# Optimization experiments

Hardware: AMD Instinct MI355X
Metric: run time of the kernel (lower is better)

## Reference

```python
import jax, jax.numpy as jnp
import numpy as np

P_CLAMP = 10.0      # opt.p
OUTPUT_SCALE = 0.1  # opt.output_scale
S_LR = 0.1          # s_lr passed to step()
R_DIM, C_DIM, HID, NLAYERS = 8192, 2048, 20, 2


def _lstm_one_step(x, h0, c0, layers):
    # x: (B, 1) single-time-step input; h0, c0: (NLAYERS, B, HID)
    # torch gate order: i, f, g, o
    inp = x
    for l, (Wih, Whh, bih, bhh) in enumerate(layers):
        gates = inp @ Wih.T + bih + h0[l] @ Whh.T + bhh  # (B, 4H)
        i, f, g, o = jnp.split(gates, 4, axis=-1)
        c = jax.nn.sigmoid(f) * c0[l] + jax.nn.sigmoid(i) * jnp.tanh(g)
        inp = jax.nn.sigmoid(o) * jnp.tanh(c)
    return inp  # last-layer hidden state (B, HID)


def _orth_proj(M, G):
    # tangent projection on the Stiefel manifold
    A = M.T @ G                      # (c, c)
    A_sym = 0.5 * (A + A.T)
    return G - M @ A_sym


def _retraction(M, P):
    Q, R = jnp.linalg.qr(M + P)      # reduced QR, M+P is (r, c), r >= c
    sign = jnp.sign(jnp.sign(jnp.diagonal(R)) + 0.5)  # maps 0 -> +1
    return Q * sign[None, :]


def _log_sign_diag(gram_diag):
    # diagonal of LogAndSign_Preprocess_Gradient: clamp(log|x|/p, -1, 1)
    return jnp.clip(jnp.log(jnp.abs(gram_diag)) / P_CLAMP, -1.0, 1.0)[:, None]


def reference(s, s_grad, L_h0, L_c0, R_h0, R_c0, L_before, R_before,
              W_ih0, W_hh0, b_ih0, b_hh0, W_ih1, W_hh1, b_ih1, b_hh1,
              L_W, L_b, R_W, R_b):
    s0 = s.shape[0]
    M = s.reshape(s0, -1).T                   # (r, c)
    M_grad = s_grad.reshape(s0, -1).T * S_LR  # (r, c)
    r, c = M.shape
    G = _orth_proj(M, M_grad)
    # only the diagonals of GG^T/c and G^TG/r are ever used by the preprocess
    ggt_diag = jnp.sum(G * G, axis=1) / c     # (r,)
    gtg_diag = jnp.sum(G * G, axis=0) / r     # (c,)
    layers = [(W_ih0, W_hh0, b_ih0, b_hh0), (W_ih1, W_hh1, b_ih1, b_hh1)]
    hl = _lstm_one_step(_log_sign_diag(ggt_diag), L_h0, L_c0, layers)  # (r, H)
    hr = _lstm_one_step(_log_sign_diag(gtg_diag), R_h0, R_c0, layers)  # (c, H)
    l_ = (hl @ L_W.T + L_b).squeeze(-1) * OUTPUT_SCALE
    l_ = l_ - l_.mean() + 1.0
    r_ = (hr @ R_W.T + R_b).squeeze(-1) * OUTPUT_SCALE
    r_ = r_ - r_.mean() + 1.0
    Lv = jnp.maximum(l_, L_before)            # diag matrices stored as vectors
    Rv = jnp.maximum(r_, R_before)
    P = Lv[:, None] * G * Rv[None, :]         # L @ G @ R with diagonal L, R
    P = _orth_proj(M, P)
    new_s = _retraction(M, -P).T.reshape(s.shape)
    return new_s


def setup_inputs() -> dict:
    key = jax.random.key(0)
    ks = jax.random.split(key, 16)
    H4 = 4 * HID
    return {
        "s": jax.random.normal(ks[0], (C_DIM, R_DIM), jnp.float32) * 0.02,
        "s_grad": jax.random.normal(ks[1], (C_DIM, R_DIM), jnp.float32) * 0.02,
        "L_h0": jax.random.normal(ks[2], (NLAYERS, R_DIM, HID), jnp.float32) * 0.1,
        "L_c0": jax.random.normal(ks[3], (NLAYERS, R_DIM, HID), jnp.float32) * 0.1,
        "R_h0": jax.random.normal(ks[4], (NLAYERS, C_DIM, HID), jnp.float32) * 0.1,
        "R_c0": jax.random.normal(ks[5], (NLAYERS, C_DIM, HID), jnp.float32) * 0.1,
        "L_before": jnp.ones((R_DIM,), jnp.float32),
        "R_before": jnp.ones((C_DIM,), jnp.float32),
        "W_ih0": jax.random.normal(ks[6], (H4, 1), jnp.float32) * 0.2,
        "W_hh0": jax.random.normal(ks[7], (H4, HID), jnp.float32) * 0.2,
        "b_ih0": jax.random.normal(ks[8], (H4,), jnp.float32) * 0.1,
        "b_hh0": jax.random.normal(ks[9], (H4,), jnp.float32) * 0.1,
        "W_ih1": jax.random.normal(ks[10], (H4, HID), jnp.float32) * 0.2,
        "W_hh1": jax.random.normal(ks[11], (H4, HID), jnp.float32) * 0.2,
        "b_ih1": jax.random.normal(ks[12], (H4,), jnp.float32) * 0.1,
        "b_hh1": jax.random.normal(ks[13], (H4,), jnp.float32) * 0.1,
        "L_W": jax.random.normal(ks[14], (1, HID), jnp.float32) * 0.2,
        "L_b": jnp.zeros((1,), jnp.float32),
        "R_W": jax.random.normal(ks[15], (1, HID), jnp.float32) * 0.2,
        "R_b": jnp.zeros((1,), jnp.float32),
    }
```

## Files before the change

### kernel.cpp

```cpp
#include <hip/hip_runtime.h>
#include <math.h>

#define RD 8192
#define CD 2048

typedef _Float16 f16x8 __attribute__((ext_vector_type(8)));
typedef _Float16 f16x4 __attribute__((ext_vector_type(4)));
typedef float    f32x4 __attribute__((ext_vector_type(4)));

#define GLOBAL_AS __attribute__((address_space(1)))
#define LDS_AS    __attribute__((address_space(3)))

__global__ __launch_bounds__(512, 2) void gemm_nt_f16(
    const _Float16* __restrict__ A, const _Float16* __restrict__ B,
    float* __restrict__ Cp, _Float16* __restrict__ Of16,
    const float* __restrict__ Dg, const _Float16* __restrict__ Eg,
    int M, int N, int K, int ksplit, float beta, float gamma, float sgn)
{
  __shared__ __align__(1024) _Float16 As[2][256 * 32];
  __shared__ __align__(1024) _Float16 Bs[2][256 * 32];
  const int tid = threadIdx.x;
  const int wave = tid >> 6, lane = tid & 63;
  const int wy = wave >> 2, wx = wave & 3;
  const int bi = blockIdx.y * 256, bj = blockIdx.x * 256;
  const int kchunk = K / ksplit;
  const long k0 = (long)blockIdx.z * kchunk;

  f32x4 acc[8][4];
#pragma unroll
  for (int i = 0; i < 8; ++i)
#pragma unroll
    for (int j = 0; j < 4; ++j) acc[i][j] = (f32x4){0.f, 0.f, 0.f, 0.f};

  const int srow = wave * 16 + (lane >> 2);
  const int skof = (lane & 3) * 8;
  const _Float16* aA = A + (long)(bi + srow) * K + k0 + skof;
  const _Float16* aB = B + (long)(bj + srow) * K + k0 + skof;
  const int ldso = wave * 16 * 32;

#define STAGE(buf, kt)                                                         \
  {                                                                            \
    _Float16* lA = &As[buf][ldso];                                             \
    _Float16* lB = &Bs[buf][ldso];                                             \
    _Pragma("unroll")                                                          \
    for (int q = 0; q < 2; ++q) {                                              \
      __builtin_amdgcn_global_load_lds(                                        \
          (const GLOBAL_AS unsigned int*)(aA + (long)q * 128 * K + (kt)),      \
          (LDS_AS unsigned int*)(lA + q * 128 * 32), 16, 0, 0);                \
      __builtin_amdgcn_global_load_lds(                                        \
          (const GLOBAL_AS unsigned int*)(aB + (long)q * 128 * K + (kt)),      \
          (LDS_AS unsigned int*)(lB + q * 128 * 32), 16, 0, 0);                \
    }                                                                          \
  }

  const int fr = lane & 15;
  const int fk = (lane >> 4) * 8;

  STAGE(0, 0);
  __syncthreads();
  int cur = 0;
  for (int kt = 0; kt < kchunk; kt += 32) {
    if (kt + 32 < kchunk) STAGE(cur ^ 1, kt + 32);

    f16x8 af[8], bf[4];
#pragma unroll
    for (int t = 0; t < 8; ++t)
      af[t] = *(const f16x8*)(&As[cur][(wy * 128 + t * 16 + fr) * 32 + fk]);
#pragma unroll
    for (int t = 0; t < 4; ++t)
      bf[t] = *(const f16x8*)(&Bs[cur][(wx * 64 + t * 16 + fr) * 32 + fk]);
#pragma unroll
    for (int mt = 0; mt < 8; ++mt)
#pragma unroll
      for (int nt = 0; nt < 4; ++nt)
        acc[mt][nt] = __builtin_amdgcn_mfma_f32_16x16x32_f16(af[mt], bf[nt], acc[mt][nt], 0, 0, 0);

    __syncthreads();
    cur ^= 1;
  }
#undef STAGE

  const int quad = lane >> 4, fc = lane & 15;
  if (Cp) {
#pragma unroll
    for (int mt = 0; mt < 8; ++mt)
#pragma unroll
      for (int nt = 0; nt < 4; ++nt) {
        const int col = bj + wx * 64 + nt * 16 + fc;
#pragma unroll
        for (int reg = 0; reg < 4; ++reg) {
          const int row = bi + wy * 128 + mt * 16 + quad * 4 + reg;
          atomicAdd(&Cp[(long)row * N + col], acc[mt][nt][reg]);
        }
      }
  } else {
#pragma unroll
    for (int mt = 0; mt < 8; ++mt)
#pragma unroll
      for (int nt = 0; nt < 4; ++nt) {
        const int col = bj + wx * 64 + nt * 16 + fc;
#pragma unroll
        for (int reg = 0; reg < 4; ++reg) {
          const int row = bi + wy * 128 + mt * 16 + quad * 4 + reg;
          const long off = (long)row * N + col;
          float v = sgn * acc[mt][nt][reg];
          if (Dg) v += beta * Dg[off];
          if (Eg) v += gamma * (float)Eg[off];
          Of16[off] = (_Float16)v;
        }
      }
  }
}

__global__ __launch_bounds__(256) void sym_combine(
    const float* __restrict__ Cp, float* __restrict__ out, int n, int nsplit, float scale)
{
  __shared__ float Ts[64][68];
  const int tid = threadIdx.x;
  const int tx = tid & 15, ty = tid >> 4;
  const int bi = blockIdx.y * 64, bj = blockIdx.x * 64;
  float acc[4][4];
#pragma unroll
  for (int i = 0; i < 4; ++i)
#pragma unroll
    for (int j = 0; j < 4; ++j) acc[i][j] = 0.f;

  for (int s = 0; s < nsplit; ++s) {
    const float* C = Cp + (long)s * n * n;
#pragma unroll
    for (int i = 0; i < 4; ++i) {
      float4 v = *(const float4*)(C + (long)(bi + ty * 4 + i) * n + bj + tx * 4);
      acc[i][0] += v.x; acc[i][1] += v.y; acc[i][2] += v.z; acc[i][3] += v.w;
    }
    __syncthreads();
#pragma unroll
    for (int i = 0; i < 4; ++i) {
      float4 w = *(const float4*)(C + (long)(bj + ty * 4 + i) * n + bi + tx * 4);
      *(float4*)&Ts[ty * 4 + i][tx * 4] = w;
    }
    __syncthreads();
#pragma unroll
    for (int i = 0; i < 4; ++i)
#pragma unroll
      for (int j = 0; j < 4; ++j) acc[i][j] += Ts[tx * 4 + j][ty * 4 + i];
  }
#pragma unroll
  for (int i = 0; i < 4; ++i) {
    float4 v; v.x = scale * acc[i][0]; v.y = scale * acc[i][1]; v.z = scale * acc[i][2]; v.w = scale * acc[i][3];
    *(float4*)(out + (long)(bi + ty * 4 + i) * n + bj + tx * 4) = v;
  }
}

__global__ __launch_bounds__(256) void cast_f16(const float* __restrict__ s, _Float16* __restrict__ d)
{
  const long i = ((long)blockIdx.x * 256 + threadIdx.x) * 4;
  float4 v = *(const float4*)(s + i);
  f16x4 o; o[0] = (_Float16)v.x; o[1] = (_Float16)v.y; o[2] = (_Float16)v.z; o[3] = (_Float16)v.w;
  *(f16x4*)(d + i) = o;
}

__global__ __launch_bounds__(256) void cast_f32(const _Float16* __restrict__ s, float* __restrict__ d)
{
  const long i = ((long)blockIdx.x * 256 + threadIdx.x) * 8;
  f16x8 v = *(const f16x8*)(s + i);
  float4 a, b;
  a.x = (float)v[0]; a.y = (float)v[1]; a.z = (float)v[2]; a.w = (float)v[3];
  b.x = (float)v[4]; b.y = (float)v[5]; b.z = (float)v[6]; b.w = (float)v[7];
  *(float4*)(d + i) = a;
  *(float4*)(d + i + 4) = b;
}

__global__ __launch_bounds__(256) void transpose_cast_f16(
    const float* __restrict__ src, _Float16* __restrict__ dst)
{
  __shared__ float T[64][65];
  const int tid = threadIdx.x, tx = tid & 15, ty = tid >> 4;
  const int r0 = blockIdx.x * 64, c0 = blockIdx.y * 64;
#pragma unroll
  for (int i = 0; i < 4; ++i) {
    float4 v = *(const float4*)(src + (long)(c0 + ty * 4 + i) * RD + r0 + tx * 4);
    T[ty * 4 + i][tx * 4 + 0] = v.x; T[ty * 4 + i][tx * 4 + 1] = v.y;
    T[ty * 4 + i][tx * 4 + 2] = v.z; T[ty * 4 + i][tx * 4 + 3] = v.w;
  }
  __syncthreads();
#pragma unroll
  for (int i = 0; i < 4; ++i) {
    f16x4 o;
#pragma unroll
    for (int j = 0; j < 4; ++j) o[j] = (_Float16)T[tx * 4 + j][ty * 4 + i];
    *(f16x4*)(dst + (long)(r0 + ty * 4 + i) * CD + c0 + tx * 4) = o;
  }
}

__global__ __launch_bounds__(256) void transpose_f16(
    const _Float16* __restrict__ src, _Float16* __restrict__ dst)
{
  __shared__ _Float16 T[64][72];
  const int tid = threadIdx.x;
  const int r0 = blockIdx.y * 64;
  const int c0 = blockIdx.x * 64;
  const int sr = tid >> 2, sc = (tid & 3) * 16;
  {
    f16x8 a = *(const f16x8*)(src + (long)(r0 + sr) * RD + c0 + sc);
    f16x8 b = *(const f16x8*)(src + (long)(r0 + sr) * RD + c0 + sc + 8);
    *(f16x8*)&T[sr][sc] = a;
    *(f16x8*)&T[sr][sc + 8] = b;
  }
  __syncthreads();
  {
    f16x8 a, b;
#pragma unroll
    for (int q = 0; q < 8; ++q) { a[q] = T[sc + q][sr]; b[q] = T[sc + 8 + q][sr]; }
    *(f16x8*)(dst + (long)(c0 + sr) * CD + r0 + sc) = a;
    *(f16x8*)(dst + (long)(c0 + sr) * CD + r0 + sc + 8) = b;
  }
}

__global__ __launch_bounds__(256) void row_sumsq(const _Float16* __restrict__ G, float* __restrict__ out, float inv)
{
  __shared__ float red[256];
  const int tid = threadIdx.x;
  const _Float16* row = G + (long)blockIdx.x * RD;
  float s = 0.f;
  for (int c = tid * 8; c < RD; c += 2048) {
    f16x8 v = *(const f16x8*)(row + c);
#pragma unroll
    for (int u = 0; u < 8; ++u) { float f = (float)v[u]; s += f * f; }
  }
  red[tid] = s; __syncthreads();
  for (int off = 128; off > 0; off >>= 1) { if (tid < off) red[tid] += red[tid + off]; __syncthreads(); }
  if (tid == 0) out[blockIdx.x] = red[0] * inv;
}

__global__ __launch_bounds__(256) void col_sumsq(const _Float16* __restrict__ G, float* __restrict__ out)
{
  const int rr = blockIdx.x * 256 + threadIdx.x;
  const int cc0 = blockIdx.y * 256;
  float s = 0.f;
  for (int i = 0; i < 256; ++i) {
    float v = (float)G[(long)(cc0 + i) * RD + rr];
    s += v * v;
  }
  atomicAdd(&out[rr], s * (1.f / (float)CD));
}

__device__ __forceinline__ float sigm_(float x) { return 1.f / (1.f + __expf(-x)); }
__device__ __forceinline__ float tanh_(float x) { float e = __expf(2.f * x); return 1.f - 2.f / (e + 1.f); }

__global__ __launch_bounds__(256) void lstm_head(
    const float* __restrict__ diag, int B,
    const float* __restrict__ h0, const float* __restrict__ c0,
    const float* __restrict__ Wih0, const float* __restrict__ Whh0,
    const float* __restrict__ bih0, const float* __restrict__ bhh0,
    const float* __restrict__ Wih1, const float* __restrict__ Whh1,
    const float* __restrict__ bih1, const float* __restrict__ bhh1,
    const float* __restrict__ HW, const float* __restrict__ Hb,
    float* __restrict__ pre, float* __restrict__ sum_out)
{
  __shared__ float w0[80], wh0[1600], b0[80], wi1[1600], wh1[1600], b1[80], hw[20];
  __shared__ float red[256];
  const int tid = threadIdx.x;
  for (int i = tid; i < 80; i += 256) { w0[i] = Wih0[i]; b0[i] = bih0[i] + bhh0[i]; b1[i] = bih1[i] + bhh1[i]; }
  for (int i = tid; i < 1600; i += 256) { wh0[i] = Whh0[i]; wi1[i] = Wih1[i]; wh1[i] = Whh1[i]; }
  if (tid < 20) hw[tid] = HW[tid];
  __syncthreads();

  const int b = blockIdx.x * 256 + tid;
  const float d = diag[b];
  float x = logf(fabsf(d)) * 0.1f;
  x = fminf(fmaxf(x, -1.f), 1.f);

  const float* h0p = h0 + (long)b * 20;
  const float* c0p = c0 + (long)b * 20;
  const float* h1p = h0 + (long)B * 20 + (long)b * 20;
  const float* c1p = c0 + (long)B * 20 + (long)b * 20;

  float h0r[20], hA[20];
#pragma unroll
  for (int m = 0; m < 20; ++m) h0r[m] = h0p[m];
#pragma unroll
  for (int h = 0; h < 20; ++h) {
    float gi = w0[h] * x + b0[h];
    float gf = w0[20 + h] * x + b0[20 + h];
    float gg = w0[40 + h] * x + b0[40 + h];
    float go = w0[60 + h] * x + b0[60 + h];
#pragma unroll
    for (int m = 0; m < 20; ++m) {
      const float hm = h0r[m];
      gi += wh0[h * 20 + m] * hm;
      gf += wh0[(20 + h) * 20 + m] * hm;
      gg += wh0[(40 + h) * 20 + m] * hm;
      go += wh0[(60 + h) * 20 + m] * hm;
    }
    const float cc = sigm_(gf) * c0p[h] + sigm_(gi) * tanh_(gg);
    hA[h] = sigm_(go) * tanh_(cc);
  }
  float h1r[20];
#pragma unroll
  for (int m = 0; m < 20; ++m) h1r[m] = h1p[m];
  float pr = 0.f;
#pragma unroll
  for (int h = 0; h < 20; ++h) {
    float gi = b1[h], gf = b1[20 + h], gg = b1[40 + h], go = b1[60 + h];
#pragma unroll
    for (int m = 0; m < 20; ++m) {
      const float am = hA[m], hm = h1r[m];
      gi += wi1[h * 20 + m] * am + wh1[h * 20 + m] * hm;
      gf += wi1[(20 + h) * 20 + m] * am + wh1[(20 + h) * 20 + m] * hm;
      gg += wi1[(40 + h) * 20 + m] * am + wh1[(40 + h) * 20 + m] * hm;
      go += wi1[(60 + h) * 20 + m] * am + wh1[(60 + h) * 20 + m] * hm;
    }
    const float cc = sigm_(gf) * c1p[h] + sigm_(gi) * tanh_(gg);
    pr += sigm_(go) * tanh_(cc) * hw[h];
  }
  pr = (pr + Hb[0]) * 0.1f;
  pre[b] = pr;

  red[tid] = pr; __syncthreads();
  for (int off = 128; off > 0; off >>= 1) { if (tid < off) red[tid] += red[tid + off]; __syncthreads(); }
  if (tid == 0) atomicAdd(sum_out, red[0]);
}

__global__ __launch_bounds__(256) void scale_P(
    _Float16* __restrict__ G, const float* __restrict__ lpre, const float* __restrict__ rpre,
    const float* __restrict__ Lbef, const float* __restrict__ Rbef, const float* __restrict__ sums)
{
  const long id4 = ((long)blockIdx.x * 256 + threadIdx.x) * 4;
  const int cc = (int)(id4 >> 13);
  const int rr = (int)(id4 & (RD - 1));
  const float meanl = sums[0] * (1.f / (float)RD);
  const float meanr = sums[1] * (1.f / (float)CD);
  const float rv = fmaxf(rpre[cc] - meanr + 1.f, Rbef[cc]);
  f16x4 g = *(f16x4*)(G + id4);
  float4 lp = *(const float4*)(lpre + rr);
  float4 lb = *(const float4*)(Lbef + rr);
  g[0] = (_Float16)((float)g[0] * rv * fmaxf(lp.x - meanl + 1.f, lb.x));
  g[1] = (_Float16)((float)g[1] * rv * fmaxf(lp.y - meanl + 1.f, lb.y));
  g[2] = (_Float16)((float)g[2] * rv * fmaxf(lp.z - meanl + 1.f, lb.z));
  g[3] = (_Float16)((float)g[3] * rv * fmaxf(lp.w - meanl + 1.f, lb.w));
  *(f16x4*)(G + id4) = g;
}

__device__ __forceinline__ void potrf_block_dev(
    float* __restrict__ S, float* __restrict__ W, float* __restrict__ KinvA,
    int d, int kprev, float (*Ls)[68], float (*Ws)[68], float (*Ts)[68])
{
  const int tid = threadIdx.x;
  const int tx = tid & 15, ty = tid >> 4;
  const long dofs = (long)d * 64;

  for (int t = tid; t < 4096; t += 256) {
    int r = t >> 6, c = t & 63;
    Ls[r][c] = S[(dofs + r) * CD + dofs + c];
  }

  if (kprev >= 0) {
    const float* Kp = KinvA + (long)kprev * 4096;
    const long ko = (long)kprev * 64;
    for (int t = tid; t < 4096; t += 256) {
      int r = t >> 6, c = t & 63;
      Ts[r][c] = S[(dofs + r) * CD + ko + c];
      Ws[r][c] = Kp[t];
    }
    __syncthreads();
    float u[4][4];
#pragma unroll
    for (int i = 0; i < 4; ++i)
#pragma unroll
      for (int j = 0; j < 4; ++j) u[i][j] = 0.f;
    for (int m = 0; m < 64; ++m) {
      float a[4], k2[4];
#pragma unroll
      for (int q = 0; q < 4; ++q) { a[q] = Ts[ty * 4 + q][m]; k2[q] = Ws[m][tx * 4 + q]; }
#pragma unroll
      for (int i = 0; i < 4; ++i)
#pragma unroll
        for (int j = 0; j < 4; ++j) u[i][j] += a[i] * k2[j];
    }
    __syncthreads();
#pragma unroll
    for (int i = 0; i < 4; ++i)
#pragma unroll
      for (int j = 0; j < 4; ++j) Ws[ty * 4 + i][tx * 4 + j] = u[i][j];
    __syncthreads();
    float acc[4][4];
#pragma unroll
    for (int i = 0; i < 4; ++i)
#pragma unroll
      for (int j = 0; j < 4; ++j) acc[i][j] = 0.f;
    for (int m = 0; m < 64; ++m) {
      float a[4], b2[4];
#pragma unroll
      for (int q = 0; q < 4; ++q) { a[q] = Ws[ty * 4 + q][m]; b2[q] = Ts[tx * 4 + q][m]; }
#pragma unroll
      for (int i = 0; i < 4; ++i)
#pragma unroll
        for (int j = 0; j < 4; ++j) acc[i][j] += a[i] * b2[j];
    }
#pragma unroll
    for (int i = 0; i < 4; ++i)
#pragma unroll
      for (int j = 0; j < 4; ++j) Ls[ty * 4 + i][tx * 4 + j] -= acc[i][j];
  }

  for (int j = 0; j < 64; ++j) {
    __syncthreads();
    const float invd = 1.f / Ls[j][j];
    for (int i = j + 1 + ty; i < 64; i += 16) {
      const float vi = Ls[i][j] * invd;
      for (int c = j + 1 + tx; c <= i; c += 16)
        Ls[i][c] -= vi * Ls[c][j];
    }
  }
  __syncthreads();
  if (tid < 64) Ts[0][tid] = 1.f / sqrtf(Ls[tid][tid]);
  __syncthreads();
  for (int t = tid; t < 4096; t += 256) {
    int r = t >> 6, c = t & 63;
    if (c <= r) Ls[r][c] *= Ts[0][c];
  }
  for (int t = tid; t < 4096; t += 256) { int r = t >> 6, c = t & 63; Ws[r][c] = 0.f; }
  __syncthreads();

  {
    const int w = tid >> 6, l = tid & 63;
    if (l < 16) {
      const int o = w * 16, c = l;
      float wr[16];
#pragma unroll
      for (int m = 0; m < 16; ++m) {
        float s = 0.f;
#pragma unroll
        for (int k = 0; k < m; ++k) s += Ls[o + m][o + k] * wr[k];
        const float rli = 1.f / Ls[o + m][o + m];
        wr[m] = (m == c) ? rli : -s * rli;
      }
#pragma unroll
      for (int m = 0; m < 16; ++m) Ws[o + m][o + c] = (m < c) ? 0.f : wr[m];
    }
  }
  __syncthreads();

  {
    for (int e = tid; e < 512; e += 256) {
      const int p = e >> 8, m = (e >> 4) & 15, c = e & 15, b0 = p * 32;
      float s = 0.f;
#pragma unroll
      for (int k = 0; k < 16; ++k) s += Ls[b0 + 16 + m][b0 + k] * Ws[b0 + k][b0 + c];
      Ts[p * 16 + m][c] = s;
    }
    __syncthreads();
    for (int e = tid; e < 512; e += 256) {
      const int p = e >> 8, m = (e >> 4) & 15, c = e & 15, b0 = p * 32;
      float s = 0.f;
#pragma unroll
      for (int k = 0; k < 16; ++k) s += Ws[b0 + 16 + m][b0 + 16 + k] * Ts[p * 16 + k][c];
      Ws[b0 + 16 + m][b0 + c] = -s;
    }
  }
  __syncthreads();

  {
    for (int q = 0; q < 4; ++q) {
      const int e = tid + 256 * q, m = e >> 5, c = e & 31;
      float s = 0.f;
#pragma unroll
      for (int k = 0; k < 32; ++k) s += Ls[32 + m][k] * Ws[k][c];
      Ts[m][c] = s;
    }
    __syncthreads();
    for (int q = 0; q < 4; ++q) {
      const int e = tid + 256 * q, m = e >> 5, c = e & 31;
      float s = 0.f;
#pragma unroll
      for (int k = 0; k < 32; ++k) s += Ws[32 + m][32 + k] * Ts[k][c];
      Ws[32 + m][c] = -s;
    }
  }
  __syncthreads();

  for (int t = tid; t < 4096; t += 256) {
    int r = t >> 6, c = t & 63;
    W[(dofs + r) * 2048 + dofs + c] = Ws[r][c];
  }
  {
    float acc[4][4];
#pragma unroll
    for (int i = 0; i < 4; ++i)
#pragma unroll
      for (int j = 0; j < 4; ++j) acc[i][j] = 0.f;
    for (int m = 0; m < 64; ++m) {
      float a[4], b2[4];
#pragma unroll
      for (int q = 0; q < 4; ++q) { a[q] = Ws[m][ty * 4 + q]; b2[q] = Ws[m][tx * 4 + q]; }
#pragma unroll
      for (int i = 0; i < 4; ++i)
#pragma unroll
        for (int j = 0; j < 4; ++j) acc[i][j] += a[i] * b2[j];
    }
    float* Kd = KinvA + (long)d * 4096;
#pragma unroll
    for (int i = 0; i < 4; ++i)
#pragma unroll
      for (int j = 0; j < 4; ++j)
        Kd[(ty * 4 + i) * 64 + tx * 4 + j] = acc[i][j];
  }
}

__global__ __launch_bounds__(256) void potrf_seed(
    float* __restrict__ S, float* __restrict__ W, float* __restrict__ KinvA)
{
  __shared__ float Ls[64][68];
  __shared__ float Ws[64][68];
  __shared__ float Ts[64][68];
  potrf_block_dev(S, W, KinvA, 0, -1, Ls, Ws, Ts);
}

__global__ __launch_bounds__(256) void ptstep_f(
    float* __restrict__ S, float* __restrict__ W, float* __restrict__ KinvA, int kb)
{
  __shared__ float As[64][68];
  __shared__ float Bs[64][68];
  __shared__ float Ts[64][68];
  const int tid = threadIdx.x, tx = tid & 15, ty = tid >> 4;
  const long ko = (long)kb * 64;
  const int nrem = 31 - kb;

  if (blockIdx.y == (unsigned)(nrem + 1)) {
    if (blockIdx.x != 0) return;
    potrf_block_dev(S, W, KinvA, kb + 1, kb, As, Bs, Ts);
    return;
  }

  if (blockIdx.y == 0) {
    const int ib = kb + 1 + blockIdx.x;
    const long ro = (long)ib * 64;
    for (int t = tid; t < 4096; t += 256) {
      int r = t >> 6, c = t & 63;
      As[r][c] = S[(ro + r) * CD + ko + c];
      Bs[r][c] = W[(ko + r) * 2048 + ko + c];
    }
    __syncthreads();
    float acc[4][4];
#pragma unroll
    for (int i = 0; i < 4; ++i)
#pragma unroll
      for (int j = 0; j < 4; ++j) acc[i][j] = 0.f;
    for (int m = 0; m < 64; ++m) {
      float a[4], w[4];
#pragma unroll
      for (int q = 0; q < 4; ++q) { a[q] = As[ty * 4 + q][m]; w[q] = Bs[tx * 4 + q][m]; }
#pragma unroll
      for (int i = 0; i < 4; ++i)
#pragma unroll
        for (int j = 0; j < 4; ++j) acc[i][j] += a[i] * w[j];
    }
#pragma unroll
    for (int i = 0; i < 4; ++i)
#pragma unroll
      for (int j = 0; j < 4; ++j)
        S[(ko + tx * 4 + j) * CD + ro + ty * 4 + i] = acc[i][j];
  } else {
    const int ib = kb + blockIdx.y;
    const int jb = kb + 1 + blockIdx.x;
    if (jb > ib) return;
    if (blockIdx.y == 1 && blockIdx.x == 0) return;
    const long io = (long)ib * 64, jo = (long)jb * 64;
    const float* Kp = KinvA + (long)kb * 4096;
    for (int t = tid; t < 4096; t += 256) {
      int r = t >> 6, c = t & 63;
      As[r][c] = S[(io + r) * CD + ko + c];
      Bs[r][c] = Kp[t];
    }
    __syncthreads();
    float acc[4][4];
#pragma unroll
    for (int i = 0; i < 4; ++i)
#pragma unroll
      for (int j = 0; j < 4; ++j) acc[i][j] = 0.f;
    for (int m = 0; m < 64; ++m) {
      float a[4], k2[4];
#pragma unroll
      for (int q = 0; q < 4; ++q) { a[q] = As[ty * 4 + q][m]; k2[q] = Bs[m][tx * 4 + q]; }
#pragma unroll
      for (int i = 0; i < 4; ++i)
#pragma unroll
        for (int j = 0; j < 4; ++j) acc[i][j] += a[i] * k2[j];
    }
#pragma unroll
    for (int i = 0; i < 4; ++i)
#pragma unroll
      for (int j = 0; j < 4; ++j) Ts[ty * 4 + i][tx * 4 + j] = acc[i][j];
    __syncthreads();
    for (int t = tid; t < 4096; t += 256) {
      int r = t >> 6, c = t & 63;
      Bs[r][c] = S[(jo + r) * CD + ko + c];
    }
    __syncthreads();
    float acc2[4][4];
#pragma unroll
    for (int i = 0; i < 4; ++i)
#pragma unroll
      for (int j = 0; j < 4; ++j) acc2[i][j] = 0.f;
    for (int m = 0; m < 64; ++m) {
      float t2[4], b2[4];
#pragma unroll
      for (int q = 0; q < 4; ++q) { t2[q] = Ts[ty * 4 + q][m]; b2[q] = Bs[tx * 4 + q][m]; }
#pragma unroll
      for (int i = 0; i < 4; ++i)
#pragma unroll
        for (int j = 0; j < 4; ++j) acc2[i][j] += t2[i] * b2[j];
    }
#pragma unroll
    for (int i = 0; i < 4; ++i)
#pragma unroll
      for (int j = 0; j < 4; ++j)
        S[(io + ty * 4 + i) * CD + jo + tx * 4 + j] -= acc2[i][j];
  }
}

__global__ __launch_bounds__(256) void winv_tn(
    const float* __restrict__ S, const float* __restrict__ W, float* __restrict__ T, int s)
{
  __shared__ float Ua[16][68];
  __shared__ float Wa[16][68];
  const int tid = threadIdx.x, tx = tid & 15, ty = tid >> 4;
  const int p = blockIdx.z, b = 2 * p * s;
  const int i0 = blockIdx.y * 64, j0 = blockIdx.x * 64;
  const int sr = tid >> 4, sc = (tid & 15) * 4;
  float acc[4][4];
#pragma unroll
  for (int i = 0; i < 4; ++i)
#pragma unroll
    for (int j = 0; j < 4; ++j) acc[i][j] = 0.f;

  for (int k0 = 0; k0 < s; k0 += 16) {
    __syncthreads();
    {
      float4 u = *(const float4*)(S + (long)(b + k0 + sr) * CD + (b + s) + i0 + sc);
      *(float4*)&Ua[sr][sc] = u;
      float4 w = *(const float4*)(W + (long)(b + k0 + sr) * 2048 + b + j0 + sc);
      *(float4*)&Wa[sr][sc] = w;
    }
    __syncthreads();
#pragma unroll
    for (int kk = 0; kk < 16; ++kk) {
      float a[4], w2[4];
#pragma unroll
      for (int q = 0; q < 4; ++q) { a[q] = Ua[kk][ty * 4 + q]; w2[q] = Wa[kk][tx * 4 + q]; }
#pragma unroll
      for (int i = 0; i < 4; ++i)
#pragma unroll
        for (int j = 0; j < 4; ++j) acc[i][j] += a[i] * w2[j];
    }
  }
  float* Tp = T + (long)p * s * s;
#pragma unroll
  for (int i = 0; i < 4; ++i)
#pragma unroll
    for (int j = 0; j < 4; ++j)
      Tp[(long)(i0 + ty * 4 + i) * s + j0 + tx * 4 + j] = acc[i][j];
}

__global__ __launch_bounds__(256) void winv_nn(
    float* __restrict__ W, const float* __restrict__ T, int s)
{
  __shared__ float Wc[64][20];
  __shared__ float Tt[16][68];
  const int tid = threadIdx.x, tx = tid & 15, ty = tid >> 4;
  const int p = blockIdx.z, b = 2 * p * s, bs = b + s;
  const int i0 = blockIdx.y * 64, j0 = blockIdx.x * 64;
  const float* Tp = T + (long)p * s * s;
  float acc[4][4];
#pragma unroll
  for (int i = 0; i < 4; ++i)
#pragma unroll
    for (int j = 0; j < 4; ++j) acc[i][j] = 0.f;

  for (int k0 = 0; k0 < s; k0 += 16) {
    __syncthreads();
    {
      const int wr = tid >> 2, wc = (tid & 3) * 4;
      float4 a = *(const float4*)(W + (long)(bs + i0 + wr) * 2048 + bs + k0 + wc);
      *(float4*)&Wc[wr][wc] = a;
      const int tr = tid >> 4, tc = (tid & 15) * 4;
      float4 t2 = *(const float4*)(Tp + (long)(k0 + tr) * s + j0 + tc);
      *(float4*)&Tt[tr][tc] = t2;
    }
    __syncthreads();
#pragma unroll
    for (int kk = 0; kk < 16; ++kk) {
      float a[4], t3[4];
#pragma unroll
      for (int q = 0; q < 4; ++q) { a[q] = Wc[ty * 4 + q][kk]; t3[q] = Tt[kk][tx * 4 + q]; }
#pragma unroll
      for (int i = 0; i < 4; ++i)
#pragma unroll
        for (int j = 0; j < 4; ++j) acc[i][j] += a[i] * t3[j];
    }
  }
#pragma unroll
  for (int i = 0; i < 4; ++i)
#pragma unroll
    for (int j = 0; j < 4; ++j)
      W[(long)(bs + i0 + ty * 4 + i) * 2048 + b + j0 + tx * 4 + j] = -acc[i][j];
}

extern "C" void kernel_launch(void* const* d_in, const int* in_sizes, int n_in,
                              void* d_out, int out_size, void* d_ws, size_t ws_size,
                              hipStream_t stream)
{
  const float* s_in  = (const float*)d_in[0];
  const float* sgrad = (const float*)d_in[1];
  const float* L_h0  = (const float*)d_in[2];
  const float* L_c0  = (const float*)d_in[3];
  const float* R_h0  = (const float*)d_in[4];
  const float* R_c0  = (const float*)d_in[5];
  const float* L_bef = (const float*)d_in[6];
  const float* R_bef = (const float*)d_in[7];
  const float* Wih0  = (const float*)d_in[8];
  const float* Whh0  = (const float*)d_in[9];
  const float* bih0  = (const float*)d_in[10];
  const float* bhh0  = (const float*)d_in[11];
  const float* Wih1  = (const float*)d_in[12];
  const float* Whh1  = (const float*)d_in[13];
  const float* bih1  = (const float*)d_in[14];
  const float* bhh1  = (const float*)d_in[15];
  const float* L_W   = (const float*)d_in[16];
  const float* L_b   = (const float*)d_in[17];
  const float* R_W   = (const float*)d_in[18];
  const float* R_b   = (const float*)d_in[19];

  float* out = (float*)d_out;
  char*  ws  = (char*)d_ws;

  const size_t SYM_OFF = (size_t)1 << 17;
  const size_t OVL_OFF = SYM_OFF + ((size_t)16 << 20);
  const size_t BIG_OFF = OVL_OFF + ((size_t)32 << 20);
  float* vec  = (float*)ws;
  float* sums = vec;
  float* ggt  = vec + 4;
  float* gtg  = ggt + RD;
  float* lpre = gtg + CD;
  float* rpre = lpre + RD;
  float*     SYM  = (float*)(ws + SYM_OFF);
  float*     Cp   = (float*)(ws + OVL_OFF);
  _Float16*  SYMh = (_Float16*)(ws + OVL_OFF);
  float*     Wf   = (float*)(ws + OVL_OFF + ((size_t)1 << 20));
  _Float16*  Wh   = (_Float16*)(ws + OVL_OFF + ((size_t)17 << 20));
  float*     Tbuf = (float*)(ws + OVL_OFF + ((size_t)25 << 20));
  float*     KinvA= (float*)(ws + OVL_OFF + ((size_t)29 << 20));
  _Float16*  BIG  = (_Float16*)(ws + BIG_OFF);

  _Float16* Mt_h  = (_Float16*)d_out;
  _Float16* slotB = Mt_h + (long)CD * RD;
  _Float16* Xtr   = (_Float16*)d_out;

  hipMemsetAsync(vec, 0, (4 + RD) * sizeof(float), stream);
  hipMemsetAsync(Cp, 0, (size_t)CD * CD * sizeof(float), stream);

  const dim3 blk(256);
  const dim3 blkG(512);
  const dim3 gK8(8, 8, 4);
  const dim3 gK2(32, 8, 1);
  const dim3 gSym(32, 32);
  const int  castBlocks = (CD * RD / 4) / 256;

  cast_f16<<<castBlocks, blk, 0, stream>>>(s_in, Mt_h);
  cast_f16<<<castBlocks, blk, 0, stream>>>(sgrad, slotB);

  gemm_nt_f16<<<gK8, blkG, 0, stream>>>(Mt_h, slotB, Cp, nullptr, nullptr, nullptr,
                                        CD, CD, RD, 4, 0.f, 0.f, 1.f);
  sym_combine<<<gSym, blk, 0, stream>>>(Cp, SYM, CD, 1, 0.05f);
  cast_f16<<<(CD * CD / 4) / 256, blk, 0, stream>>>(SYM, SYMh);

  transpose_cast_f16<<<dim3(RD / 64, CD / 64), blk, 0, stream>>>(s_in, slotB);

  gemm_nt_f16<<<gK2, blkG, 0, stream>>>(SYMh, slotB, nullptr, BIG, sgrad, nullptr,
                                        CD, RD, CD, 1, 0.1f, 0.f, -1.f);

  row_sumsq<<<CD, blk, 0, stream>>>(BIG, gtg, 1.f / (float)RD);
  col_sumsq<<<dim3(RD / 256, CD / 256), blk, 0, stream>>>(BIG, ggt);

  lstm_head<<<RD / 256, blk, 0, stream>>>(ggt, RD, L_h0, L_c0, Wih0, Whh0, bih0, bhh0,
                                          Wih1, Whh1, bih1, bhh1, L_W, L_b, lpre, &sums[0]);
  lstm_head<<<CD / 256, blk, 0, stream>>>(gtg, CD, R_h0, R_c0, Wih0, Whh0, bih0, bhh0,
                                          Wih1, Whh1, bih1, bhh1, R_W, R_b, rpre, &sums[1]);

  scale_P<<<(CD * (RD / 4)) / 256, blk, 0, stream>>>(BIG, lpre, rpre, L_bef, R_bef, sums);

  hipMemsetAsync(Cp, 0, (size_t)CD * CD * sizeof(float), stream);
  gemm_nt_f16<<<gK8, blkG, 0, stream>>>(Mt_h, BIG, Cp, nullptr, nullptr, nullptr,
                                        CD, CD, RD, 4, 0.f, 0.f, 1.f);
  sym_combine<<<gSym, blk, 0, stream>>>(Cp, SYM, CD, 1, 0.5f);
  cast_f16<<<(CD * CD / 4) / 256, blk, 0, stream>>>(SYM, SYMh);

  gemm_nt_f16<<<gK2, blkG, 0, stream>>>(SYMh, slotB, nullptr, BIG, s_in, BIG,
                                        CD, RD, CD, 1, 1.f, -1.f, 1.f);

  hipMemsetAsync(Cp, 0, (size_t)CD * CD * sizeof(float), stream);
  gemm_nt_f16<<<gK8, blkG, 0, stream>>>(BIG, BIG, Cp, nullptr, nullptr, nullptr,
                                        CD, CD, RD, 4, 0.f, 0.f, 1.f);
  sym_combine<<<gSym, blk, 0, stream>>>(Cp, SYM, CD, 1, 0.5f);

  hipMemsetAsync(Wf, 0, (size_t)CD * CD * sizeof(float), stream);
  transpose_f16<<<dim3(RD / 64, CD / 64), blk, 0, stream>>>(BIG, Xtr);

  potrf_seed<<<1, blk, 0, stream>>>(SYM, Wf, KinvA);
  for (int kb = 0; kb < 31; ++kb) {
    const int nrem = 31 - kb;
    ptstep_f<<<dim3(nrem, nrem + 2), blk, 0, stream>>>(SYM, Wf, KinvA, kb);
  }

  for (int lev = 0; lev < 5; ++lev) {
    const int s = 64 << lev, npairs = 16 >> lev;
    const dim3 g(s / 64, s / 64, npairs);
    winv_tn<<<g, blk, 0, stream>>>(SYM, Wf, Tbuf, s);
    winv_nn<<<g, blk, 0, stream>>>(Wf, Tbuf, s);
  }

  cast_f16<<<(CD * CD / 4) / 256, blk, 0, stream>>>(Wf, Wh);
  gemm_nt_f16<<<gK2, blkG, 0, stream>>>(Wh, Xtr, nullptr, BIG, nullptr, nullptr,
                                        CD, RD, CD, 1, 0.f, 0.f, 1.f);
  cast_f32<<<(CD * RD / 8) / 256, blk, 0, stream>>>(BIG, out);
}
```

Before: 3.090 ms.

## Deepen GEMM K-tile with swizzled LDS, exploit symmetry in X^TX, fuse f16 cast

The f16 GEMM now stages 64-wide K tiles with an XOR-swizzled LDS layout, which is meant to avoid bank conflicts. Its main loop is split into four barrier-separated MFMA phases that interleave the next tile's loads and raise wave priority around the MFMAs. For the symmetric BIG^T·BIG product, only the lower-triangle blocks are computed, and sym_combine mirrors the missing half. sym_combine can also write f16 output directly, which removes the separate cast kernels. The larger LDS footprint (128KB per block) may lower occupancy, and the many extra barriers add synchronisation cost.

Result: faster. 2.938 ms (-4.9%).

```diff
diff --git a/kernel.cpp b/kernel.cpp
--- a/kernel.cpp
+++ b/kernel.cpp
@@ -15,10 +15,12 @@
     const _Float16* __restrict__ A, const _Float16* __restrict__ B,
     float* __restrict__ Cp, _Float16* __restrict__ Of16,
     const float* __restrict__ Dg, const _Float16* __restrict__ Eg,
-    int M, int N, int K, int ksplit, float beta, float gamma, float sgn)
-{
-  __shared__ __align__(1024) _Float16 As[2][256 * 32];
-  __shared__ __align__(1024) _Float16 Bs[2][256 * 32];
+    int M, int N, int K, int ksplit, int tri, float beta, float gamma, float sgn)
+{
+  if (tri && blockIdx.x > blockIdx.y) return;
+
+  __shared__ __align__(1024) _Float16 As[2][256 * 64];
+  __shared__ __align__(1024) _Float16 Bs[2][256 * 64];
   const int tid = threadIdx.x;
   const int wave = tid >> 6, lane = tid & 63;
   const int wy = wave >> 2, wx = wave & 3;
@@ -32,53 +34,85 @@
 #pragma unroll
     for (int j = 0; j < 4; ++j) acc[i][j] = (f32x4){0.f, 0.f, 0.f, 0.f};
 
-  const int srow = wave * 16 + (lane >> 2);
-  const int skof = (lane & 3) * 8;
-  const _Float16* aA = A + (long)(bi + srow) * K + k0 + skof;
-  const _Float16* aB = B + (long)(bj + srow) * K + k0 + skof;
-  const int ldso = wave * 16 * 32;
-
-#define STAGE(buf, kt)                                                         \
+  const _Float16* aAb = A + (long)bi * K + k0;
+  const _Float16* aBb = B + (long)bj * K + k0;
+  const int fr = lane & 15;
+  const int hi = lane >> 4;
+
+#define STAGE_H(gb, Xs, buf, h, kt)                                            \
   {                                                                            \
-    _Float16* lA = &As[buf][ldso];                                             \
-    _Float16* lB = &Bs[buf][ldso];                                             \
     _Pragma("unroll")                                                          \
     for (int q = 0; q < 2; ++q) {                                              \
+      const int idx = q * 512 + tid;                                           \
+      const int row = idx >> 3, cc = idx & 7;                                  \
+      const int cs = cc ^ (row & 7);                                           \
       __builtin_amdgcn_global_load_lds(                                        \
-          (const GLOBAL_AS unsigned int*)(aA + (long)q * 128 * K + (kt)),      \
-          (LDS_AS unsigned int*)(lA + q * 128 * 32), 16, 0, 0);                \
-      __builtin_amdgcn_global_load_lds(                                        \
-          (const GLOBAL_AS unsigned int*)(aB + (long)q * 128 * K + (kt)),      \
-          (LDS_AS unsigned int*)(lB + q * 128 * 32), 16, 0, 0);                \
+          (const GLOBAL_AS unsigned int*)(gb + (long)((h) * 128 + row) * K + (kt) + cs * 8), \
+          (LDS_AS unsigned int*)(&Xs[buf][(h) * 8192 + q * 4096 + wave * 512]),\
+          16, 0, 0);                                                           \
     }                                                                          \
   }
 
-  const int fr = lane & 15;
-  const int fk = (lane >> 4) * 8;
-
-  STAGE(0, 0);
-  __syncthreads();
-  int cur = 0;
-  for (int kt = 0; kt < kchunk; kt += 32) {
-    if (kt + 32 < kchunk) STAGE(cur ^ 1, kt + 32);
-
-    f16x8 af[8], bf[4];
-#pragma unroll
-    for (int t = 0; t < 8; ++t)
-      af[t] = *(const f16x8*)(&As[cur][(wy * 128 + t * 16 + fr) * 32 + fk]);
-#pragma unroll
-    for (int t = 0; t < 4; ++t)
-      bf[t] = *(const f16x8*)(&Bs[cur][(wx * 64 + t * 16 + fr) * 32 + fk]);
-#pragma unroll
-    for (int mt = 0; mt < 8; ++mt)
-#pragma unroll
-      for (int nt = 0; nt < 4; ++nt)
-        acc[mt][nt] = __builtin_amdgcn_mfma_f32_16x16x32_f16(af[mt], bf[nt], acc[mt][nt], 0, 0, 0);
-
-    __syncthreads();
-    cur ^= 1;
-  }
-#undef STAGE
+#define LDA4(mh, kk)                                                           \
+  _Pragma("unroll")                                                            \
+  for (int j = 0; j < 4; ++j) {                                                \
+    const int rA = wy * 128 + ((mh) * 4 + j) * 16 + fr;                        \
+    af[j] = *(const f16x8*)(&As[cur][rA * 64 + (((kk) * 4 + hi) ^ (rA & 7)) * 8]); \
+  }
+#define LDB4(kk)                                                               \
+  _Pragma("unroll")                                                            \
+  for (int j = 0; j < 4; ++j) {                                                \
+    const int rB = wx * 64 + j * 16 + fr;                                      \
+    bf[j] = *(const f16x8*)(&Bs[cur][rB * 64 + (((kk) * 4 + hi) ^ (rB & 7)) * 8]); \
+  }
+#define MFMA16(mh)                                                             \
+  _Pragma("unroll")                                                            \
+  for (int j = 0; j < 4; ++j)                                                  \
+    _Pragma("unroll")                                                          \
+    for (int n2 = 0; n2 < 4; ++n2)                                             \
+      acc[(mh) * 4 + j][n2] = __builtin_amdgcn_mfma_f32_16x16x32_f16(          \
+          af[j], bf[n2], acc[(mh) * 4 + j][n2], 0, 0, 0);
+
+  const int nt_ = kchunk >> 6;
+
+  STAGE_H(aAb, As, 0, 0, 0); STAGE_H(aAb, As, 0, 1, 0);
+  STAGE_H(aBb, Bs, 0, 0, 0); STAGE_H(aBb, Bs, 0, 1, 0);
+  asm volatile("s_waitcnt vmcnt(0)" ::: "memory");
+  __syncthreads();
+
+  for (int t = 0; t < nt_; ++t) {
+    const int cur = t & 1, nxt = cur ^ 1;
+    const int ktn = (t + 1) << 6;
+    const bool more = (t + 1 < nt_);
+    f16x8 af[4], bf[4];
+
+    LDB4(0); LDA4(0, 0);
+    if (more) { STAGE_H(aAb, As, nxt, 0, ktn); STAGE_H(aAb, As, nxt, 1, ktn); }
+    __builtin_amdgcn_s_barrier();
+    __builtin_amdgcn_s_setprio(1); MFMA16(0); __builtin_amdgcn_s_setprio(0);
+    __builtin_amdgcn_s_barrier();
+
+    LDA4(1, 0);
+    if (more) { STAGE_H(aBb, Bs, nxt, 0, ktn); STAGE_H(aBb, Bs, nxt, 1, ktn); }
+    __builtin_amdgcn_s_barrier();
+    __builtin_amdgcn_s_setprio(1); MFMA16(1); __builtin_amdgcn_s_setprio(0);
+    __builtin_amdgcn_s_barrier();
+
+    LDB4(1); LDA4(0, 1);
+    __builtin_amdgcn_s_barrier();
+    __builtin_amdgcn_s_setprio(1); MFMA16(0); __builtin_amdgcn_s_setprio(0);
+    __builtin_amdgcn_s_barrier();
+
+    LDA4(1, 1);
+    __builtin_amdgcn_s_barrier();
+    __builtin_amdgcn_s_setprio(1); MFMA16(1); __builtin_amdgcn_s_setprio(0);
+    asm volatile("s_waitcnt vmcnt(0)" ::: "memory");
+    __builtin_amdgcn_s_barrier();
+  }
+#undef STAGE_H
+#undef LDA4
+#undef LDB4
+#undef MFMA16
 
   const int quad = lane >> 4, fc = lane & 15;
   if (Cp) {
@@ -113,7 +147,8 @@
 }
 
 __global__ __launch_bounds__(256) void sym_combine(
-    const float* __restrict__ Cp, float* __restrict__ out, int n, int nsplit, float scale)
+    const float* __restrict__ Cp, float* __restrict__ outf, _Float16* __restrict__ outh,
+    int n, int mirror, float scale)
 {
   __shared__ float Ts[64][68];
   const int tid = threadIdx.x;
@@ -125,17 +160,15 @@
 #pragma unroll
     for (int j = 0; j < 4; ++j) acc[i][j] = 0.f;
 
-  for (int s = 0; s < nsplit; ++s) {
-    const float* C = Cp + (long)s * n * n;
+  if (!mirror) {
 #pragma unroll
     for (int i = 0; i < 4; ++i) {
-      float4 v = *(const float4*)(C + (long)(bi + ty * 4 + i) * n + bj + tx * 4);
+      float4 v = *(const float4*)(Cp + (long)(bi + ty * 4 + i) * n + bj + tx * 4);
       acc[i][0] += v.x; acc[i][1] += v.y; acc[i][2] += v.z; acc[i][3] += v.w;
     }
-    __syncthreads();
 #pragma unroll
     for (int i = 0; i < 4; ++i) {
-      float4 w = *(const float4*)(C + (long)(bj + ty * 4 + i) * n + bi + tx * 4);
+      float4 w = *(const float4*)(Cp + (long)(bj + ty * 4 + i) * n + bi + tx * 4);
       *(float4*)&Ts[ty * 4 + i][tx * 4] = w;
     }
     __syncthreads();
@@ -143,11 +176,35 @@
     for (int i = 0; i < 4; ++i)
 #pragma unroll
       for (int j = 0; j < 4; ++j) acc[i][j] += Ts[tx * 4 + j][ty * 4 + i];
+  } else if (bi >= bj) {
+#pragma unroll
+    for (int i = 0; i < 4; ++i) {
+      float4 v = *(const float4*)(Cp + (long)(bi + ty * 4 + i) * n + bj + tx * 4);
+      acc[i][0] = 2.f * v.x; acc[i][1] = 2.f * v.y; acc[i][2] = 2.f * v.z; acc[i][3] = 2.f * v.w;
+    }
+  } else {
+#pragma unroll
+    for (int i = 0; i < 4; ++i) {
+      float4 w = *(const float4*)(Cp + (long)(bj + ty * 4 + i) * n + bi + tx * 4);
+      *(float4*)&Ts[ty * 4 + i][tx * 4] = w;
+    }
+    __syncthreads();
+#pragma unroll
+    for (int i = 0; i < 4; ++i)
+#pragma unroll
+      for (int j = 0; j < 4; ++j) acc[i][j] = 2.f * Ts[tx * 4 + j][ty * 4 + i];
   }
 #pragma unroll
   for (int i = 0; i < 4; ++i) {
-    float4 v; v.x = scale * acc[i][0]; v.y = scale * acc[i][1]; v.z = scale * acc[i][2]; v.w = scale * acc[i][3];
-    *(float4*)(out + (long)(bi + ty * 4 + i) * n + bj + tx * 4) = v;
+    const long off = (long)(bi + ty * 4 + i) * n + bj + tx * 4;
+    float4 v; v.x = scale * acc[i][0]; v.y = scale * acc[i][1];
+    v.z = scale * acc[i][2]; v.w = scale * acc[i][3];
+    if (outf) *(float4*)(outf + off) = v;
+    if (outh) {
+      f16x4 h; h[0] = (_Float16)v.x; h[1] = (_Float16)v.y;
+      h[2] = (_Float16)v.z; h[3] = (_Float16)v.w;
+      *(f16x4*)(outh + off) = h;
+    }
   }
 }
 
@@ -744,8 +801,8 @@
   float* lpre = gtg + CD;
   float* rpre = lpre + RD;
   float*     SYM  = (float*)(ws + SYM_OFF);
+  _Float16*  SYMh = (_Float16*)(ws + SYM_OFF);
   float*     Cp   = (float*)(ws + OVL_OFF);
-  _Float16*  SYMh = (_Float16*)(ws + OVL_OFF);
   float*     Wf   = (float*)(ws + OVL_OFF + ((size_t)1 << 20));
   _Float16*  Wh   = (_Float16*)(ws + OVL_OFF + ((size_t)17 << 20));
   float*     Tbuf = (float*)(ws + OVL_OFF + ((size_t)25 << 20));
@@ -770,14 +827,13 @@
   cast_f16<<<castBlocks, blk, 0, stream>>>(sgrad, slotB);
 
   gemm_nt_f16<<<gK8, blkG, 0, stream>>>(Mt_h, slotB, Cp, nullptr, nullptr, nullptr,
-                                        CD, CD, RD, 4, 0.f, 0.f, 1.f);
-  sym_combine<<<gSym, blk, 0, stream>>>(Cp, SYM, CD, 1, 0.05f);
-  cast_f16<<<(CD * CD / 4) / 256, blk, 0, stream>>>(SYM, SYMh);
+                                        CD, CD, RD, 4, 0, 0.f, 0.f, 1.f);
+  sym_combine<<<gSym, blk, 0, stream>>>(Cp, nullptr, SYMh, CD, 0, 0.05f);
 
   transpose_cast_f16<<<dim3(RD / 64, CD / 64), blk, 0, stream>>>(s_in, slotB);
 
   gemm_nt_f16<<<gK2, blkG, 0, stream>>>(SYMh, slotB, nullptr, BIG, sgrad, nullptr,
-                                        CD, RD, CD, 1, 0.1f, 0.f, -1.f);
+                                        CD, RD, CD, 1, 0, 0.1f, 0.f, -1.f);
 
   row_sumsq<<<CD, blk, 0, stream>>>(BIG, gtg, 1.f / (float)RD);
   col_sumsq<<<dim3(RD / 256, CD / 256), blk, 0, stream>>>(BIG, ggt);
@@ -791,17 +847,16 @@
 
   hipMemsetAsync(Cp, 0, (size_t)CD * CD * sizeof(float), stream);
   gemm_nt_f16<<<gK8, blkG, 0, stream>>>(Mt_h, BIG, Cp, nullptr, nullptr, nullptr,
-                                        CD, CD, RD, 4, 0.f, 0.f, 1.f);
-  sym_combine<<<gSym, blk, 0, stream>>>(Cp, SYM, CD, 1, 0.5f);
-  cast_f16<<<(CD * CD / 4) / 256, blk, 0, stream>>>(SYM, SYMh);
+                                        CD, CD, RD, 4, 0, 0.f, 0.f, 1.f);
+  sym_combine<<<gSym, blk, 0, stream>>>(Cp, nullptr, SYMh, CD, 0, 0.5f);
 
   gemm_nt_f16<<<gK2, blkG, 0, stream>>>(SYMh, slotB, nullptr, BIG, s_in, BIG,
-                                        CD, RD, CD, 1, 1.f, -1.f, 1.f);
+                                        CD, RD, CD, 1, 0, 1.f, -1.f, 1.f);
 
   hipMemsetAsync(Cp, 0, (size_t)CD * CD * sizeof(float), stream);
   gemm_nt_f16<<<gK8, blkG, 0, stream>>>(BIG, BIG, Cp, nullptr, nullptr, nullptr,
-                                        CD, CD, RD, 4, 0.f, 0.f, 1.f);
-  sym_combine<<<gSym, blk, 0, stream>>>(Cp, SYM, CD, 1, 0.5f);
+                                        CD, CD, RD, 4, 1, 0.f, 0.f, 1.f);
+  sym_combine<<<gSym, blk, 0, stream>>>(Cp, SYM, nullptr, CD, 1, 0.5f);
 
   hipMemsetAsync(Wf, 0, (size_t)CD * CD * sizeof(float), stream);
   transpose_f16<<<dim3(RD / 64, CD / 64), blk, 0, stream>>>(BIG, Xtr);
@@ -821,6 +876,6 @@
 
   cast_f16<<<(CD * CD / 4) / 256, blk, 0, stream>>>(Wf, Wh);
   gemm_nt_f16<<<gK2, blkG, 0, stream>>>(Wh, Xtr, nullptr, BIG, nullptr, nullptr,
-                                        CD, RD, CD, 1, 0.f, 0.f, 1.f);
+                                        CD, RD, CD, 1, 0, 0.f, 0.f, 1.f);
   cast_f32<<<(CD * RD / 8) / 256, blk, 0, stream>>>(BIG, out);
 }
```
